# Optimization experiments

Hardware: AMD Instinct MI355X
Metric: run time of the kernel (lower is better)

The kernel has to match this reference:

```python
import jax, jax.numpy as jnp
import numpy as np

N_PATHS = 512   # n: Monte-Carlo simulation paths
N_STEPS = 32    # m: Euler-Maruyama time steps
B_OPTS  = 64    # number of option contracts (len(S0))
HID     = 64    # hidden width of each of the 4 MLPs
V0      = 0.2   # initial volatility
RHO     = -0.7  # Brownian correlation


def setup_inputs() -> dict:
    key = jax.random.key(0)
    ks = jax.random.split(key, 10)
    S0 = jax.random.uniform(ks[0], (B_OPTS,), minval=50.0, maxval=150.0, dtype=jnp.float32)
    K  = jax.random.uniform(ks[1], (B_OPTS,), minval=50.0, maxval=150.0, dtype=jnp.float32)
    T  = jax.random.uniform(ks[2], (B_OPTS,), minval=0.25, maxval=2.0, dtype=jnp.float32)
    rf = jnp.float32(0.03)
    Z1 = jax.random.normal(ks[3], (N_PATHS, N_STEPS), dtype=jnp.float32)
    Z2 = RHO * Z1 + np.sqrt(1.0 - RHO ** 2).astype(np.float32) * jax.random.normal(ks[4], (N_PATHS, N_STEPS), dtype=jnp.float32)
    # 4 structurally-identical MLPs [4 -> HID -> HID -> 1], stacked on a leading net axis
    s0 = 1.0 / np.sqrt(4.0); s1 = 1.0 / np.sqrt(HID)
    W0 = jax.random.normal(ks[5], (4, 4, HID), dtype=jnp.float32) * s0
    b0 = jnp.zeros((4, HID), dtype=jnp.float32)
    W1 = jax.random.normal(ks[6], (4, HID, HID), dtype=jnp.float32) * s1
    b1 = jnp.zeros((4, HID), dtype=jnp.float32)
    W2 = jax.random.normal(ks[7], (4, HID, 1), dtype=jnp.float32) * s1
    b2 = jnp.zeros((4, 1), dtype=jnp.float32)
    return dict(S0=S0, K=K, T=T, rf=rf, Z1=Z1, Z2=Z2, W0=W0, b0=b0, W1=W1, b1=b1, W2=W2, b2=b2)


def _mlp(x, w0, c0, w1, c1, w2, c2):
    # x: (n, B, 4) -> (n, B, 1); tanh MLP as in class NN
    h = jnp.tanh(x @ w0 + c0)
    h = jnp.tanh(h @ w1 + c1)
    return h @ w2 + c2


def reference(S0, K, T, rf, Z1, Z2, W0, b0, W1, b1, W2, b2):
    n, m = Z1.shape
    Bn = S0.shape[0]
    dt = T / m                                    # (B,)
    ndt = jnp.broadcast_to(dt[None, :, None], (n, Bn, 1))
    nrf = jnp.full((n, Bn, 1), rf, dtype=jnp.float32)
    sqrt_ndt = jnp.sqrt(ndt)
    S_init = jnp.broadcast_to(S0[None, :, None], (n, Bn, 1)) * jnp.ones((n, 1, 1), jnp.float32)
    V_init = jnp.full((n, Bn, 1), V0, dtype=jnp.float32)

    def step(carry, xs):
        S, V = carry
        j, z1, z2 = xs                            # z1, z2: (n,)
        tcol = ndt * j
        inp = jnp.concatenate([S, V, nrf, tcol], axis=2)   # (n, B, 4)
        S = S * (1.0
                 + _mlp(inp, W0[0], b0[0], W1[0], b1[0], W2[0], b2[0]) * ndt
                 + _mlp(inp, W0[1], b0[1], W1[1], b1[1], W2[1], b2[1]) * z1[:, None, None])
        inp2 = jnp.concatenate([S, V, nrf, tcol], axis=2)  # uses UPDATED S, as in source
        V = V * (1.0
                 + _mlp(inp2, W0[2], b0[2], W1[2], b1[2], W2[2], b2[2]) * ndt
                 + _mlp(inp2, W0[3], b0[3], W1[3], b1[3], W2[3], b2[3]) * sqrt_ndt * z2[:, None, None])
        return (S, V), None

    xs = (jnp.arange(m, dtype=jnp.float32), Z1.T, Z2.T)
    (S, V), _ = jax.lax.scan(step, (S_init, V_init), xs)

    Sq = S[..., 0]                                # (n, B)
    P_future = jnp.where(Sq - K[None, :] < 0, jnp.float32(0.0), Sq)
    P_pred = jnp.sum(jnp.exp(-rf * T)[None, :] * P_future, axis=0) / n
    return P_pred
```

## Files before the change

### kernel.cpp

```cpp
#include <hip/hip_runtime.h>


#define N_PATHS 512
#define N_STEPS 32
#define B_OPTS  64
#define HID     64

#define TANH_K 2.8853900817779268f

typedef __attribute__((ext_vector_type(8))) short bf16x8;
typedef __attribute__((ext_vector_type(4))) float f32x4;
typedef __attribute__((ext_vector_type(4))) unsigned u32x4;

__device__ __forceinline__ float tanh_from_scaled(float a) {
    float u = __builtin_amdgcn_exp2f(a);
    float r = __builtin_amdgcn_rcpf(u + 1.0f);
    return fmaf(-2.0f, r, 1.0f);
}

__device__ __forceinline__ short f2bf(float f) {
    union { float f; unsigned u; } c; c.f = f;
    unsigned u = c.u + 0x7FFFu + ((c.u >> 16) & 1u);
    return (short)(u >> 16);
}

__device__ __forceinline__ unsigned cvt_pk_bf16(float lo, float hi) {
    unsigned r;
    asm("v_cvt_pk_bf16_f32 %0, %1, %2" : "=v"(r) : "v"(lo), "v"(hi));
    return r;
}

__device__ __forceinline__ float mlp_one(
    int net, int q, int nh,
    float Sa, float Va, float tA,
    const float4* __restrict__ w0t4,
    const uint4*  __restrict__ w1p,
    const float*  __restrict__ b1k,
    const float (&w2v)[4][4], float b2s)
{
    asm volatile("" ::: "memory");
    uint4 wfr[8];
#pragma unroll
    for (int i = 0; i < 8; ++i) wfr[i] = w1p[(net * 8 + i) * 64];

    u32x4 afr[2];
#pragma unroll
    for (int kh = 0; kh < 2; ++kh) {
        float tv[8];
#pragma unroll
        for (int j = 0; j < 8; ++j) {
            const int kk = kh * 32 + q * 8 + j;
            const float4 w = w0t4[net * 72 + kk + (kk >> 3)];
            const float a = fmaf(Sa, w.x, fmaf(Va, w.y, fmaf(tA, w.z, w.w)));
            tv[j] = tanh_from_scaled(a);
        }
#pragma unroll
        for (int d = 0; d < 4; ++d)
            afr[kh][d] = cvt_pk_bf16(tv[2 * d], tv[2 * d + 1]);
    }
    const bf16x8 h0 = __builtin_bit_cast(bf16x8, afr[0]);
    const bf16x8 h1 = __builtin_bit_cast(bf16x8, afr[1]);

    float s = 0.0f;
#pragma unroll
    for (int nt = 0; nt < 4; ++nt) {
        f32x4 c = *(const f32x4*)&b1k[net * 64 + nt * 16 + 4 * q];
        c = __builtin_amdgcn_mfma_f32_16x16x32_bf16(
                __builtin_bit_cast(bf16x8, wfr[nt * 2 + 0]), h0, c, 0, 0, 0);
        c = __builtin_amdgcn_mfma_f32_16x16x32_bf16(
                __builtin_bit_cast(bf16x8, wfr[nt * 2 + 1]), h1, c, 0, 0, 0);
#pragma unroll
        for (int r = 0; r < 4; ++r)
            s = fmaf(tanh_from_scaled(c[r]), w2v[nt][r], s);
    }
    s += __shfl_xor(s, 16);
    s += __shfl_xor(s, 32);
    return s + b2s;
}

__global__ __launch_bounds__(512)
__attribute__((amdgpu_waves_per_eu(4)))
void nsde_kernel(
    const float* __restrict__ S0p, const float* __restrict__ Kp,
    const float* __restrict__ Tp,  const float* __restrict__ rfp,
    const float* __restrict__ Z1,  const float* __restrict__ Z2,
    const float* __restrict__ W0,  const float* __restrict__ b0,
    const float* __restrict__ W1,  const float* __restrict__ b1,
    const float* __restrict__ W2,  const float* __restrict__ b2,
    float* __restrict__ out, float* __restrict__ ws, int use_ws)
{
    const int tid  = threadIdx.x;
    const int wave = tid >> 6;
    const int lane = tid & 63;
    const int q    = lane >> 4;
    const int nh   = lane & 15;
    const int t    = wave >> 1;
    const int role = wave & 1;
    const int path = blockIdx.x;
    const int row  = t * 16 + nh;

    __shared__ float4 w0t4[4 * 72];
    __shared__ uint4  w1f[2048];
    __shared__ __align__(16) float b1k[4 * 64];
    __shared__ float2 fx2[64];
    __shared__ float2 gx2[64];

    const float rf = rfp[0];

    if (tid < 256) {
        const int net = tid >> 6, kk = tid & 63;
        const float wsv = W0[net * 256 + 0 * 64 + kk];
        const float wvv = W0[net * 256 + 1 * 64 + kk];
        const float wrv = W0[net * 256 + 2 * 64 + kk];
        const float wtv = W0[net * 256 + 3 * 64 + kk];
        w0t4[net * 72 + kk + (kk >> 3)] =
            make_float4(TANH_K * wsv, TANH_K * wvv, TANH_K * wtv,
                        TANH_K * fmaf(rf, wrv, b0[net * 64 + kk]));
        b1k[tid] = TANH_K * b1[tid];
    }

#pragma unroll
    for (int it = 0; it < 4; ++it) {
        const int f   = it * 512 + tid;
        const int fnh = f & 15;
        const int fq  = (f >> 4) & 3;
        const int fkh = (f >> 6) & 1;
        const int fnt = (f >> 7) & 3;
        const int fnet= (f >> 9) & 3;
        const float* wp = W1 + fnet * 4096 + (fkh * 32 + fq * 8) * 64 + fnt * 16 + fnh;
        bf16x8 fr;
#pragma unroll
        for (int j = 0; j < 8; ++j) fr[j] = f2bf(TANH_K * wp[j * 64]);
        w1f[f] = __builtin_bit_cast(uint4, fr);
    }

    const float dta  = Tp[row] * (1.0f / N_STEPS);
    const float sqdt = sqrtf(dta);
    const int netA = role;
    const int netB = role + 2;

    float w2vA[4][4], w2vB[4][4];
#pragma unroll
    for (int nt = 0; nt < 4; ++nt)
#pragma unroll
        for (int r = 0; r < 4; ++r) {
            const int hid = nt * 16 + 4 * q + r;
            w2vA[nt][r] = W2[netA * 64 + hid];
            w2vB[nt][r] = W2[netB * 64 + hid];
        }
    const float b2A = b2[netA], b2B = b2[netB];

    float Sreg = S0p[row];
    float Vreg = 0.2f;

    __syncthreads();

    const uint4* __restrict__ w1p = &w1f[q * 16 + nh];
    const float* __restrict__ z1p = Z1 + path * N_STEPS;
    const float* __restrict__ z2p = Z2 + path * N_STEPS;

    for (int step = 0; step < N_STEPS; ++step) {
        const float z1 = z1p[step];
        const float z2 = z2p[step];
        const float tA = dta * (float)step;

        const float f = mlp_one(netA, q, nh, Sreg, Vreg, tA,
                                w0t4, w1p, b1k, w2vA, b2A);
        if (q == 0) { if (role == 0) fx2[row].x = f; else fx2[row].y = f; }
        __syncthreads();
        {
            const float2 fp = fx2[row];
            Sreg = Sreg * fmaf(fp.y, z1, fmaf(fp.x, dta, 1.0f));
        }

        const float g = mlp_one(netB, q, nh, Sreg, Vreg, tA,
                                w0t4, w1p, b1k, w2vB, b2B);
        if (q == 0) { if (role == 0) gx2[row].x = g; else gx2[row].y = g; }
        __syncthreads();
        {
            const float2 gp = gx2[row];
            Vreg = Vreg * fmaf(gp.y, sqdt * z2, fmaf(gp.x, dta, 1.0f));
        }
    }

    if (role == 0 && q == 0) {
        const float Tt   = dta * (float)N_STEPS;
        const float disc = __builtin_amdgcn_exp2f(-rf * Tt * 1.4426950408889634f)
                           * (1.0f / (float)N_PATHS);
        const float Kv = Kp[row];
        const float p1 = (Sreg - Kv < 0.0f) ? 0.0f : Sreg;
        const float v  = disc * p1;
        if (use_ws) ws[path * 64 + row] = v;
        else        atomicAdd(&out[row], v);
    }
}

__global__ void reduce_kernel(const float* __restrict__ ws, float* __restrict__ out) {
    __shared__ float acc[4][64];
    const int o = threadIdx.x & 63, g = threadIdx.x >> 6;
    float s = 0.0f;
    for (int b = g; b < N_PATHS; b += 4) s += ws[b * 64 + o];
    acc[g][o] = s;
    __syncthreads();
    if (threadIdx.x < 64)
        out[threadIdx.x] = acc[0][threadIdx.x] + acc[1][threadIdx.x]
                         + acc[2][threadIdx.x] + acc[3][threadIdx.x];
}

__global__ void zero_out_kernel(float* __restrict__ out) {
    out[threadIdx.x] = 0.0f;
}

extern "C" void kernel_launch(void* const* d_in, const int* in_sizes, int n_in,
                              void* d_out, int out_size, void* d_ws, size_t ws_size,
                              hipStream_t stream) {
    const float* S0p = (const float*)d_in[0];
    const float* Kp  = (const float*)d_in[1];
    const float* Tp  = (const float*)d_in[2];
    const float* rfp = (const float*)d_in[3];
    const float* Z1  = (const float*)d_in[4];
    const float* Z2  = (const float*)d_in[5];
    const float* W0  = (const float*)d_in[6];
    const float* b0  = (const float*)d_in[7];
    const float* W1  = (const float*)d_in[8];
    const float* b1  = (const float*)d_in[9];
    const float* W2  = (const float*)d_in[10];
    const float* b2  = (const float*)d_in[11];
    float* out = (float*)d_out;
    float* wsf = (float*)d_ws;

    const int use_ws = (ws_size >= (size_t)(N_PATHS * 64 * sizeof(float))) ? 1 : 0;

    if (!use_ws) zero_out_kernel<<<1, B_OPTS, 0, stream>>>(out);
    nsde_kernel<<<N_PATHS, 512, 0, stream>>>(S0p, Kp, Tp, rfp, Z1, Z2,
                                             W0, b0, W1, b1, W2, b2, out, wsf, use_ws);
    if (use_ws) reduce_kernel<<<1, 256, 0, stream>>>(wsf, out);
}
```

Baseline: 243.8 us.

## Compute first MLP layer with bf16 MFMA using split hi/lo inputs

Replaces the scalar per-lane FMA evaluation of the 4->64 first layer with four 16x16x32 bf16 MFMAs. S and t are split into bf16 hi/lo parts and W_S and W_T into hi/lo pairs, so the K dimension carries the extra terms and keeps near-fp32 accuracy. The W1 fragment layout is re-indexed so the MFMA output layout feeds the second layer directly. This removes per-lane LDS float4 loads and FMAs, at the cost of extra LDS for zero-padded weight fragments and a longer MFMA dependency chain on the critical path.

```diff
diff --git a/kernel.cpp b/kernel.cpp
--- a/kernel.cpp
+++ b/kernel.cpp
@@ -30,10 +30,17 @@
     return r;
 }
 
+__device__ __forceinline__ void bsplit(float x, float& hi, float& lo) {
+    const unsigned u = cvt_pk_bf16(x, x);
+    hi = __builtin_bit_cast(float, u << 16);
+    lo = x - hi;
+}
+
 __device__ __forceinline__ float mlp_one(
-    int net, int q, int nh,
-    float Sa, float Va, float tA,
-    const float4* __restrict__ w0t4,
+    int net, int q,
+    bf16x8 svt,
+    const uint4*  __restrict__ w0ap,
+    const float*  __restrict__ b0e,
     const uint4*  __restrict__ w1p,
     const float*  __restrict__ b1k,
     const float (&w2v)[4][4], float b2s)
@@ -42,21 +49,28 @@
     uint4 wfr[8];
 #pragma unroll
     for (int i = 0; i < 8; ++i) wfr[i] = w1p[(net * 8 + i) * 64];
-
+    uint4 w0f[4];
+#pragma unroll
+    for (int mt = 0; mt < 4; ++mt) w0f[mt] = w0ap[(net * 4 + mt) * 64];
+
+    f32x4 c1[4];
+#pragma unroll
+    for (int mt = 0; mt < 4; ++mt) {
+        f32x4 ci = *(const f32x4*)&b0e[net * 64 + mt * 16 + 4 * q];
+        c1[mt] = __builtin_amdgcn_mfma_f32_16x16x32_bf16(
+                     __builtin_bit_cast(bf16x8, w0f[mt]), svt, ci, 0, 0, 0);
+    }
     u32x4 afr[2];
 #pragma unroll
-    for (int kh = 0; kh < 2; ++kh) {
-        float tv[8];
-#pragma unroll
-        for (int j = 0; j < 8; ++j) {
-            const int kk = kh * 32 + q * 8 + j;
-            const float4 w = w0t4[net * 72 + kk + (kk >> 3)];
-            const float a = fmaf(Sa, w.x, fmaf(Va, w.y, fmaf(tA, w.z, w.w)));
-            tv[j] = tanh_from_scaled(a);
-        }
-#pragma unroll
-        for (int d = 0; d < 4; ++d)
-            afr[kh][d] = cvt_pk_bf16(tv[2 * d], tv[2 * d + 1]);
+    for (int x = 0; x < 2; ++x) {
+        afr[x][0] = cvt_pk_bf16(tanh_from_scaled(c1[2 * x][0]),
+                                tanh_from_scaled(c1[2 * x][1]));
+        afr[x][1] = cvt_pk_bf16(tanh_from_scaled(c1[2 * x][2]),
+                                tanh_from_scaled(c1[2 * x][3]));
+        afr[x][2] = cvt_pk_bf16(tanh_from_scaled(c1[2 * x + 1][0]),
+                                tanh_from_scaled(c1[2 * x + 1][1]));
+        afr[x][3] = cvt_pk_bf16(tanh_from_scaled(c1[2 * x + 1][2]),
+                                tanh_from_scaled(c1[2 * x + 1][3]));
     }
     const bf16x8 h0 = __builtin_bit_cast(bf16x8, afr[0]);
     const bf16x8 h1 = __builtin_bit_cast(bf16x8, afr[1]);
@@ -99,8 +113,9 @@
     const int path = blockIdx.x;
     const int row  = t * 16 + nh;
 
-    __shared__ float4 w0t4[4 * 72];
+    __shared__ uint4  w0a[1024];
     __shared__ uint4  w1f[2048];
+    __shared__ __align__(16) float b0e[4 * 64];
     __shared__ __align__(16) float b1k[4 * 64];
     __shared__ float2 fx2[64];
     __shared__ float2 gx2[64];
@@ -109,14 +124,33 @@
 
     if (tid < 256) {
         const int net = tid >> 6, kk = tid & 63;
-        const float wsv = W0[net * 256 + 0 * 64 + kk];
-        const float wvv = W0[net * 256 + 1 * 64 + kk];
-        const float wrv = W0[net * 256 + 2 * 64 + kk];
-        const float wtv = W0[net * 256 + 3 * 64 + kk];
-        w0t4[net * 72 + kk + (kk >> 3)] =
-            make_float4(TANH_K * wsv, TANH_K * wvv, TANH_K * wtv,
-                        TANH_K * fmaf(rf, wrv, b0[net * 64 + kk]));
+        b0e[tid] = TANH_K * fmaf(rf, W0[net * 256 + 128 + kk], b0[tid]);
         b1k[tid] = TANH_K * b1[tid];
+    }
+
+#pragma unroll
+    for (int it = 0; it < 2; ++it) {
+        const int f   = it * 512 + tid;
+        const int ls  = f & 63;
+        const int mt  = (f >> 6) & 3;
+        const int nts = f >> 8;
+        uint4 fr = {0u, 0u, 0u, 0u};
+        if ((ls >> 4) == 0) {
+            const int H = mt * 16 + (ls & 15);
+            const float wS = TANH_K * W0[nts * 256 + 0   + H];
+            const float wV = TANH_K * W0[nts * 256 + 64  + H];
+            const float wT = TANH_K * W0[nts * 256 + 192 + H];
+            const unsigned sh = (unsigned)(unsigned short)f2bf(wS);
+            const float shf   = __builtin_bit_cast(float, sh << 16);
+            const unsigned th = (unsigned)(unsigned short)f2bf(wT);
+            const float thf   = __builtin_bit_cast(float, th << 16);
+            fr.x = sh | (sh << 16);
+            fr.y = (unsigned)(unsigned short)f2bf(wS - shf)
+                 | ((unsigned)(unsigned short)f2bf(wV) << 16);
+            fr.z = th | (th << 16);
+            fr.w = (unsigned)(unsigned short)f2bf(wT - thf);
+        }
+        w0a[f] = fr;
     }
 
 #pragma unroll
@@ -127,10 +161,12 @@
         const int fkh = (f >> 6) & 1;
         const int fnt = (f >> 7) & 3;
         const int fnet= (f >> 9) & 3;
-        const float* wp = W1 + fnet * 4096 + (fkh * 32 + fq * 8) * 64 + fnt * 16 + fnh;
         bf16x8 fr;
 #pragma unroll
-        for (int j = 0; j < 8; ++j) fr[j] = f2bf(TANH_K * wp[j * 64]);
+        for (int j = 0; j < 8; ++j) {
+            const int H = 16 * (2 * fkh + (j >> 2)) + 4 * fq + (j & 3);
+            fr[j] = f2bf(TANH_K * W1[fnet * 4096 + H * 64 + fnt * 16 + fnh]);
+        }
         w1f[f] = __builtin_bit_cast(uint4, fr);
     }
 
@@ -155,27 +191,49 @@
 
     __syncthreads();
 
-    const uint4* __restrict__ w1p = &w1f[q * 16 + nh];
-    const float* __restrict__ z1p = Z1 + path * N_STEPS;
-    const float* __restrict__ z2p = Z2 + path * N_STEPS;
+    const uint4* __restrict__ w0ap = &w0a[lane];
+    const uint4* __restrict__ w1p  = &w1f[lane];
+    const float* __restrict__ z1p  = Z1 + path * N_STEPS;
+    const float* __restrict__ z2p  = Z2 + path * N_STEPS;
+    const bool q0 = (q == 0);
 
     for (int step = 0; step < N_STEPS; ++step) {
         const float z1 = z1p[step];
         const float z2 = z2p[step];
         const float tA = dta * (float)step;
 
-        const float f = mlp_one(netA, q, nh, Sreg, Vreg, tA,
-                                w0t4, w1p, b1k, w2vA, b2A);
-        if (q == 0) { if (role == 0) fx2[row].x = f; else fx2[row].y = f; }
+        float th, tl; bsplit(tA, th, tl);
+        const unsigned td2 = cvt_pk_bf16(th, tl);
+        const unsigned td3 = cvt_pk_bf16(th, 0.0f);
+
+        {
+            float sh, sl; bsplit(Sreg, sh, sl);
+            u32x4 sv;
+            sv[0] = q0 ? cvt_pk_bf16(sh, sl)   : 0u;
+            sv[1] = q0 ? cvt_pk_bf16(sh, Vreg) : 0u;
+            sv[2] = q0 ? td2 : 0u;
+            sv[3] = q0 ? td3 : 0u;
+            const float f = mlp_one(netA, q, __builtin_bit_cast(bf16x8, sv),
+                                    w0ap, b0e, w1p, b1k, w2vA, b2A);
+            if (q0) { if (role == 0) fx2[row].x = f; else fx2[row].y = f; }
+        }
         __syncthreads();
         {
             const float2 fp = fx2[row];
             Sreg = Sreg * fmaf(fp.y, z1, fmaf(fp.x, dta, 1.0f));
         }
 
-        const float g = mlp_one(netB, q, nh, Sreg, Vreg, tA,
-                                w0t4, w1p, b1k, w2vB, b2B);
-        if (q == 0) { if (role == 0) gx2[row].x = g; else gx2[row].y = g; }
+        {
+            float sh, sl; bsplit(Sreg, sh, sl);
+            u32x4 sv;
+            sv[0] = q0 ? cvt_pk_bf16(sh, sl)   : 0u;
+            sv[1] = q0 ? cvt_pk_bf16(sh, Vreg) : 0u;
+            sv[2] = q0 ? td2 : 0u;
+            sv[3] = q0 ? td3 : 0u;
+            const float g = mlp_one(netB, q, __builtin_bit_cast(bf16x8, sv),
+                                    w0ap, b0e, w1p, b1k, w2vB, b2B);
+            if (q0) { if (role == 0) gx2[row].x = g; else gx2[row].y = g; }
+        }
         __syncthreads();
         {
             const float2 gp = gx2[row];
```

Result: no change. 240.7 us (-1.3%).
